# Kernel tuning notes

Measured on AMD Instinct MI355X. Metric: run time of the kernel, lower is better.

The kernel has to match this reference:

```python
import math
import jax, jax.numpy as jnp
import numpy as np

N, E, D, H, NH, DH, EIN, EOUT, G = 30000, 480000, 128, 128, 4, 32, 16, 16, 64
EPS = 1e-5

def _leaky(x):
    return jax.nn.leaky_relu(x, 0.01)

def _graph_norm(x, batch, w, b, a):
    # torch_geometric GraphNorm: out = w * (x - a*mean) / sqrt(var + eps) + b, stats per graph
    cnt = jnp.maximum(jax.ops.segment_sum(jnp.ones((x.shape[0],), x.dtype), batch, num_segments=G), 1.0)[:, None]
    mean = jax.ops.segment_sum(x, batch, num_segments=G) / cnt
    out = x - a * mean[batch]
    var = jax.ops.segment_sum(out * out, batch, num_segments=G) / cnt
    return w * out / jnp.sqrt(var + EPS)[batch] + b

def setup_inputs() -> dict:
    key = jax.random.key(0)
    ks = jax.random.split(key, 24)
    lin = lambda k, di, do: jax.random.normal(k, (di, do), jnp.float32) * 0.02
    z = lambda d: jnp.zeros((d,), jnp.float32)
    o = lambda d: jnp.ones((d,), jnp.float32)
    return {
        "node": jax.random.normal(ks[0], (N, D), jnp.float32),
        "edge": jax.random.normal(ks[1], (E, EIN), jnp.float32),
        "coords": jax.random.normal(ks[2], (N, 3), jnp.float32),
        "Ws": lin(ks[3], D, H), "bs": z(H),
        "Wd": lin(ks[4], D, H), "bd": z(H),
        "Wv": lin(ks[5], D, H), "bv": z(H),
        "We1": lin(ks[6], EIN + 1, H), "be1": z(H),
        "We2": lin(ks[7], H, H), "be2": z(H),
        "Wun": lin(ks[8], H, H), "bun": z(H),
        "Wue": lin(ks[9], H, EOUT), "bue": z(EOUT),
        "Wg": lin(ks[10], 3 * H, H), "bg": z(H),
        "Wf1": lin(ks[11], H, H), "bf1": z(H),
        "Wf2": lin(ks[12], H, H), "bf2": z(H),
        "gn1_w": o(H), "gn1_b": z(H), "gn1_a": o(H),
        "gn2_w": o(H), "gn2_b": z(H), "gn2_a": o(H),
        "edge_index": jax.random.randint(ks[13], (2, E), 0, N),
        "batch": jnp.sort(jax.random.randint(ks[14], (N,), 0, G)),
    }

def reference(node, edge, coords, Ws, bs, Wd, bd, Wv, bv, We1, be1, We2, be2,
              Wun, bun, Wue, bue, Wg, bg, Wf1, bf1, Wf2, bf2,
              gn1_w, gn1_b, gn1_a, gn2_w, gn2_b, gn2_a, edge_index, batch):
    i, j = edge_index[0], edge_index[1]
    src = node @ Ws + bs              # [N,H]
    dst = node @ Wd + bd
    value = node @ Wv + bv
    d = coords[i] - coords[j]
    dist = jnp.sqrt(jnp.sum(d * d, axis=-1, keepdims=True) + 1e-12) * 0.1
    e = jnp.concatenate([edge, dist], axis=-1)            # [E, EIN+1]
    e = _leaky(e @ We1 + be1) @ We2 + be2                   # edge_layer (dropout=identity in eval)
    edge_key = src[j] * e
    edge_result = (dst[i] * edge_key / math.sqrt(DH)).reshape(E, NH, DH)
    scores = jnp.sum(jnp.abs(edge_result), axis=2)         # L1 norm over dh -> [E,NH]
    smax = jax.ops.segment_max(scores, i, num_segments=N)  # scatter softmax over dst nodes
    ex = jnp.exp(scores - smax[i])
    den = jax.ops.segment_sum(ex, i, num_segments=N)
    ew = (ex / den[i])[..., None]                           # [E,NH,1]
    agg = jax.ops.segment_sum(ew * value[j].reshape(E, NH, DH), i, num_segments=N).reshape(N, H)
    node_new = agg @ Wun + bun
    edge_new = edge_result.reshape(E, H) @ Wue + bue
    g = jax.nn.sigmoid(jnp.concatenate([node_new, node, node_new - node], axis=-1) @ Wg + bg)
    n1 = _graph_norm(g * node_new + node, batch, gn1_w, gn1_b, gn1_a)
    fx = _leaky(n1 @ Wf1 + bf1) @ Wf2 + bf2                 # fix_node
    n2 = _graph_norm(g * fx + n1, batch, gn2_w, gn2_b, gn2_a)
    return (n2, edge_new, coords)
```

## Files before the change

kernel.cpp:

```cpp
#include <hip/hip_runtime.h>
#include <hip/hip_bf16.h>

#define NN_ 30000
#define NE_ 480000
#define DIM 128
#define EINF 16
#define EOUTF 16
#define NG 64
#define RSQRT_DH 0.17677669529663687f

typedef unsigned short u16;
typedef __attribute__((ext_vector_type(8))) short short8;
typedef __attribute__((ext_vector_type(8))) unsigned short ushort8v;
typedef __attribute__((ext_vector_type(4))) float floatx4;

#define W_DEG     0
#define W_CUR     30000
#define W_GSUM1   60000
#define W_GSQ1    68192
#define W_GSUM2   76384
#define W_GSQ2    84576
#define W_ZEND    92768
#define W_OFF     92768
#define W_BSUM    122772
#define W_GSTART  122900
#define W_EID     122968
#define W_JC      602968
#define W_SCORES  1082968
#define W_SRCB    3002968
#define W_DSTB    4922968
#define W_VALB    6842968
#define W_A       8762968
#define W_B       12602968
#define W_C       16442968
#define W_WGC     20282968
#define W_WE2B    20315736
#define W_WPROJ   20323928
#define W_WUEB    20455000

static __device__ __forceinline__ u16 f2bf(float x) {
  __hip_bfloat16 h = __float2bfloat16(x);
  return *reinterpret_cast<u16*>(&h);
}
static __device__ __forceinline__ float bf2f(u16 v) {
  unsigned int b = ((unsigned int)v) << 16;
  return __uint_as_float(b);
}

static __device__ __forceinline__ void tile_gn_stats(const float* xsb, int ld,
    const int* bg_s, int row0, int tid,
    float* __restrict__ gsum, float* __restrict__ gsq) {
  int c = tid & 127, half = tid >> 7;
  float sm = 0.f, sq = 0.f;
  int gcur = -1;
  for (int r = 0; r < 16; ++r) {
    int rl = half * 16 + r;
    int row = row0 + rl;
    if (row >= NN_) break;
    int g = bg_s[rl];
    float v = xsb[rl * ld + c];
    if (g != gcur) {
      if (gcur >= 0) {
        atomicAdd(&gsum[gcur * DIM + c], sm);
        atomicAdd(&gsq[gcur * DIM + c], sq);
      }
      gcur = g; sm = 0.f; sq = 0.f;
    }
    sm += v; sq += v * v;
  }
  if (gcur >= 0) {
    atomicAdd(&gsum[gcur * DIM + c], sm);
    atomicAdd(&gsq[gcur * DIM + c], sq);
  }
}

__global__ void setup_kernel(const int* __restrict__ batch, int* __restrict__ gstart,
                             const float* __restrict__ Wg,
                             const float* __restrict__ We2, u16* __restrict__ we2b,
                             const float* __restrict__ Ws, const float* __restrict__ Wd,
                             const float* __restrict__ Wv, const float* __restrict__ Wun,
                             const float* __restrict__ Wf1, const float* __restrict__ Wf2,
                             u16* __restrict__ wfrag,
                             const float* __restrict__ Wue, u16* __restrict__ wueb) {
  int b = blockIdx.x, tid = threadIdx.x;
  if (b == 0) {
    int g = tid;
    if (g <= NG) {
      int lo = 0, hi = NN_;
      while (lo < hi) { int mid = (lo + hi) >> 1; if (batch[mid] < g) lo = mid + 1; else hi = mid; }
      gstart[g] = lo;
    }
  } else if (b < 65) {
    int idx = (b - 1) * 256 + tid;
    int j = idx & 7, lane = (idx >> 3) & 63, s = (idx >> 9) & 3, T = idx >> 11;
    int k = s * 32 + ((lane >> 4) << 3) + j;
    int n = T * 16 + (lane & 15);
    we2b[idx] = f2bf(We2[(size_t)k * DIM + n]);
  } else if (b < 1089) {
    int idx = (b - 65) * 256 + tid;
    int which = idx >> 14;
    int sub = idx & 16383;
    int j = sub & 7, lane = (sub >> 3) & 63, s = (sub >> 9) & 3, T = sub >> 11;
    int k = s * 32 + ((lane >> 4) << 3) + j;
    int n = T * 16 + (lane & 15);
    int mat = which >> 1;
    float w;
    if (mat == 4) w = Wg[(size_t)k * DIM + n] + Wg[(size_t)(256 + k) * DIM + n];
    else if (mat == 5) w = Wg[(size_t)(128 + k) * DIM + n] - Wg[(size_t)(256 + k) * DIM + n];
    else {
      const float* Wsrc = (mat == 0) ? Ws : (mat == 1) ? Wd : (mat == 2) ? Wv
                        : (mat == 3) ? Wun : (mat == 6) ? Wf1 : Wf2;
      w = Wsrc[(size_t)k * DIM + n];
    }
    u16 h = f2bf(w);
    wfrag[(size_t)which * 16384 + sub] = (which & 1) ? f2bf(w - bf2f(h)) : h;
  } else {
    int idx = (b - 1089) * 256 + tid;
    int half = idx >> 12;
    int sub = idx & 4095;
    int j = sub & 7, lane = (sub >> 3) & 63, sG = sub >> 9;
    int k = sG * 32 + ((lane >> 4) << 3) + j;
    int n = lane & 15;
    float w = Wue[(size_t)k * EOUTF + n];
    u16 h = f2bf(w);
    wueb[half * 4096 + sub] = half ? f2bf(w - bf2f(h)) : h;
  }
}

__global__ void deg_kernel(const int* __restrict__ EI, int* __restrict__ deg) {
  int e = blockIdx.x * 256 + threadIdx.x;
  if (e < NE_) atomicAdd(&deg[EI[e]], 1);
}

__global__ void __launch_bounds__(256) proj_kernel(
    const float* __restrict__ node, const u16* __restrict__ wfrag,
    const float* __restrict__ bs, const float* __restrict__ bd,
    const float* __restrict__ bv,
    u16* __restrict__ srcb, u16* __restrict__ dstb, u16* __restrict__ valb) {
  __shared__ __align__(16) u16 ah[32 * 136];
  __shared__ __align__(16) u16 al[32 * 136];
  __shared__ __align__(16) float park[32 * 132];
  int tid = threadIdx.x, row0 = blockIdx.x * 32;
  int r2 = tid >> 3, c16 = (tid & 7) * 16;

  {
    int row = row0 + r2;
    float v[16];
    if (row < NN_) {
#pragma unroll
      for (int q = 0; q < 4; ++q) {
        float4 x = *(const float4*)&node[(size_t)row * DIM + c16 + q * 4];
        v[q * 4 + 0] = x.x; v[q * 4 + 1] = x.y;
        v[q * 4 + 2] = x.z; v[q * 4 + 3] = x.w;
      }
    } else {
#pragma unroll
      for (int q = 0; q < 16; ++q) v[q] = 0.f;
    }
#pragma unroll
    for (int h2 = 0; h2 < 2; ++h2) {
      ushort8v hh, ll;
#pragma unroll
      for (int q = 0; q < 8; ++q) {
        float x = v[h2 * 8 + q];
        u16 h = f2bf(x);
        hh[q] = h;
        ll[q] = f2bf(x - bf2f(h));
      }
      *(ushort8v*)&ah[r2 * 136 + c16 + h2 * 8] = hh;
      *(ushort8v*)&al[r2 * 136 + c16 + h2 * 8] = ll;
    }
  }
  __syncthreads();

  int wv_ = tid >> 6, lane = tid & 63;
  int mtile = wv_ & 1, nhalf = wv_ >> 1;
  int quad = lane >> 4, lrow = lane & 15;
  int m0 = mtile * 16;

  short8 afh[4], afl[4];
#pragma unroll
  for (int s = 0; s < 4; ++s) {
    afh[s] = *(const short8*)&ah[(m0 + lrow) * 136 + s * 32 + quad * 8];
    afl[s] = *(const short8*)&al[(m0 + lrow) * 136 + s * 32 + quad * 8];
  }

  const float* Bt[3] = {bs, bd, bv};
  u16* Yt[3] = {srcb, dstb, valb};
#pragma unroll 1
  for (int g3 = 0; g3 < 3; ++g3) {
    const u16* wh = wfrag + (size_t)(g3 * 2 + 0) * 16384;
    const u16* wl = wfrag + (size_t)(g3 * 2 + 1) * 16384;
    floatx4 dacc[4];
#pragma unroll
    for (int t = 0; t < 4; ++t) dacc[t] = (floatx4){0.f, 0.f, 0.f, 0.f};
#pragma unroll
    for (int s = 0; s < 4; ++s) {
#pragma unroll
      for (int t = 0; t < 4; ++t) {
        int T = nhalf * 4 + t;
        size_t off = (size_t)((T * 4 + s) * 64 + lane) * 8;
        short8 bh = *(const short8*)&wh[off];
        short8 bl = *(const short8*)&wl[off];
        dacc[t] = __builtin_amdgcn_mfma_f32_16x16x32_bf16(afh[s], bh, dacc[t], 0, 0, 0);
        dacc[t] = __builtin_amdgcn_mfma_f32_16x16x32_bf16(afl[s], bh, dacc[t], 0, 0, 0);
        dacc[t] = __builtin_amdgcn_mfma_f32_16x16x32_bf16(afh[s], bl, dacc[t], 0, 0, 0);
      }
    }
#pragma unroll
    for (int t = 0; t < 4; ++t) {
      int col = nhalf * 64 + t * 16 + lrow;
#pragma unroll
      for (int r = 0; r < 4; ++r)
        park[(m0 + quad * 4 + r) * 132 + col] = dacc[t][r];
    }
    __syncthreads();
    {
      int row = row0 + r2;
      if (row < NN_) {
#pragma unroll
        for (int h2 = 0; h2 < 2; ++h2) {
          ushort8v o;
#pragma unroll
          for (int q = 0; q < 8; ++q) {
            float pv = park[r2 * 132 + c16 + h2 * 8 + q] + Bt[g3][c16 + h2 * 8 + q];
            o[q] = f2bf(pv);
          }
          *(ushort8v*)&Yt[g3][(size_t)row * DIM + c16 + h2 * 8] = o;
        }
      }
    }
    __syncthreads();
  }
}

__global__ void __launch_bounds__(256) nnew_gate_kernel(
    const float* __restrict__ AGG, const float* __restrict__ NODE,
    const int* __restrict__ batch, const u16* __restrict__ wfrag,
    const float* __restrict__ bun, const float* __restrict__ bg,
    float* __restrict__ gsum1, float* __restrict__ gsq1,
    float* __restrict__ G, float* __restrict__ X1) {
  __shared__ __align__(16) u16 a_h[32 * 136];
  __shared__ __align__(16) u16 a_l[32 * 136];
  __shared__ __align__(16) u16 n_h[32 * 136];
  __shared__ __align__(16) u16 n_l[32 * 136];
  __shared__ __align__(16) float park[32 * 132];
  __shared__ int bg_s[32];
  int tid = threadIdx.x, row0 = blockIdx.x * 32;
  int r2 = tid >> 3, c16 = (tid & 7) * 16;
  if (tid < 32) bg_s[tid] = (row0 + tid < NN_) ? batch[row0 + tid] : 0;

  {
    int row = row0 + r2;
    float va[16], vn[16];
    if (row < NN_) {
#pragma unroll
      for (int q = 0; q < 4; ++q) {
        float4 xa = *(const float4*)&AGG[(size_t)row * DIM + c16 + q * 4];
        float4 xn = *(const float4*)&NODE[(size_t)row * DIM + c16 + q * 4];
        va[q * 4 + 0] = xa.x; va[q * 4 + 1] = xa.y; va[q * 4 + 2] = xa.z; va[q * 4 + 3] = xa.w;
        vn[q * 4 + 0] = xn.x; vn[q * 4 + 1] = xn.y; vn[q * 4 + 2] = xn.z; vn[q * 4 + 3] = xn.w;
      }
    } else {
#pragma unroll
      for (int q = 0; q < 16; ++q) { va[q] = 0.f; vn[q] = 0.f; }
    }
#pragma unroll
    for (int h2 = 0; h2 < 2; ++h2) {
      ushort8v ah8, al8, nh8, nl8;
#pragma unroll
      for (int q = 0; q < 8; ++q) {
        float x = va[h2 * 8 + q];
        u16 h = f2bf(x); ah8[q] = h; al8[q] = f2bf(x - bf2f(h));
        float y = vn[h2 * 8 + q];
        u16 hy = f2bf(y); nh8[q] = hy; nl8[q] = f2bf(y - bf2f(hy));
      }
      *(ushort8v*)&a_h[r2 * 136 + c16 + h2 * 8] = ah8;
      *(ushort8v*)&a_l[r2 * 136 + c16 + h2 * 8] = al8;
      *(ushort8v*)&n_h[r2 * 136 + c16 + h2 * 8] = nh8;
      *(ushort8v*)&n_l[r2 * 136 + c16 + h2 * 8] = nl8;
    }
  }
  __syncthreads();

  int wv_ = tid >> 6, lane = tid & 63;
  int mtile = wv_ & 1, nhalf = wv_ >> 1;
  int quad = lane >> 4, lrow = lane & 15;
  int m0 = mtile * 16;

  const u16* WunH = wfrag + (size_t)6 * 16384;
  const u16* WunL = wfrag + (size_t)7 * 16384;
  const u16* G0H  = wfrag + (size_t)8 * 16384;
  const u16* G0L  = wfrag + (size_t)9 * 16384;
  const u16* G1H  = wfrag + (size_t)10 * 16384;
  const u16* G1L  = wfrag + (size_t)11 * 16384;

  {
    short8 fh[4], fl[4];
#pragma unroll
    for (int s = 0; s < 4; ++s) {
      fh[s] = *(const short8*)&a_h[(m0 + lrow) * 136 + s * 32 + quad * 8];
      fl[s] = *(const short8*)&a_l[(m0 + lrow) * 136 + s * 32 + quad * 8];
    }
    floatx4 d1[4];
#pragma unroll
    for (int t = 0; t < 4; ++t) d1[t] = (floatx4){0.f, 0.f, 0.f, 0.f};
#pragma unroll
    for (int s = 0; s < 4; ++s) {
#pragma unroll
      for (int t = 0; t < 4; ++t) {
        int T = nhalf * 4 + t;
        size_t off = (size_t)((T * 4 + s) * 64 + lane) * 8;
        short8 bh = *(const short8*)&WunH[off];
        short8 bl = *(const short8*)&WunL[off];
        d1[t] = __builtin_amdgcn_mfma_f32_16x16x32_bf16(fh[s], bh, d1[t], 0, 0, 0);
        d1[t] = __builtin_amdgcn_mfma_f32_16x16x32_bf16(fl[s], bh, d1[t], 0, 0, 0);
        d1[t] = __builtin_amdgcn_mfma_f32_16x16x32_bf16(fh[s], bl, d1[t], 0, 0, 0);
      }
    }
#pragma unroll
    for (int t = 0; t < 4; ++t) {
      int col = nhalf * 64 + t * 16 + lrow;
#pragma unroll
      for (int r = 0; r < 4; ++r)
        park[(m0 + quad * 4 + r) * 132 + col] = d1[t][r];
    }
  }
  __syncthreads();

  {
#pragma unroll
    for (int h2 = 0; h2 < 2; ++h2) {
      ushort8v hh, ll;
#pragma unroll
      for (int q = 0; q < 8; ++q) {
        float x = park[r2 * 132 + c16 + h2 * 8 + q] + bun[c16 + h2 * 8 + q];
        u16 h = f2bf(x); hh[q] = h; ll[q] = f2bf(x - bf2f(h));
      }
      *(ushort8v*)&a_h[r2 * 136 + c16 + h2 * 8] = hh;
      *(ushort8v*)&a_l[r2 * 136 + c16 + h2 * 8] = ll;
    }
  }
  __syncthreads();

  {
    short8 mh[4], ml[4], ph[4], pl[4];
#pragma unroll
    for (int s = 0; s < 4; ++s) {
      mh[s] = *(const short8*)&a_h[(m0 + lrow) * 136 + s * 32 + quad * 8];
      ml[s] = *(const short8*)&a_l[(m0 + lrow) * 136 + s * 32 + quad * 8];
      ph[s] = *(const short8*)&n_h[(m0 + lrow) * 136 + s * 32 + quad * 8];
      pl[s] = *(const short8*)&n_l[(m0 + lrow) * 136 + s * 32 + quad * 8];
    }
    floatx4 d2[4];
#pragma unroll
    for (int t = 0; t < 4; ++t) d2[t] = (floatx4){0.f, 0.f, 0.f, 0.f};
#pragma unroll
    for (int s = 0; s < 4; ++s) {
#pragma unroll
      for (int t = 0; t < 4; ++t) {
        int T = nhalf * 4 + t;
        size_t off = (size_t)((T * 4 + s) * 64 + lane) * 8;
        short8 g0h = *(const short8*)&G0H[off];
        short8 g0l = *(const short8*)&G0L[off];
        short8 g1h = *(const short8*)&G1H[off];
        short8 g1l = *(const short8*)&G1L[off];
        d2[t] = __builtin_amdgcn_mfma_f32_16x16x32_bf16(mh[s], g0h, d2[t], 0, 0, 0);
        d2[t] = __builtin_amdgcn_mfma_f32_16x16x32_bf16(ml[s], g0h, d2[t], 0, 0, 0);
        d2[t] = __builtin_amdgcn_mfma_f32_16x16x32_bf16(mh[s], g0l, d2[t], 0, 0, 0);
        d2[t] = __builtin_amdgcn_mfma_f32_16x16x32_bf16(ph[s], g1h, d2[t], 0, 0, 0);
        d2[t] = __builtin_amdgcn_mfma_f32_16x16x32_bf16(pl[s], g1h, d2[t], 0, 0, 0);
        d2[t] = __builtin_amdgcn_mfma_f32_16x16x32_bf16(ph[s], g1l, d2[t], 0, 0, 0);
      }
    }
#pragma unroll
    for (int t = 0; t < 4; ++t) {
      int col = nhalf * 64 + t * 16 + lrow;
      float bgv = bg[col], bunv = bun[col];
#pragma unroll
      for (int r = 0; r < 4; ++r) {
        int erow = m0 + quad * 4 + r;
        int row = row0 + erow;
        float z = d2[t][r] + bgv;
        float gg = 1.f / (1.f + __expf(-z));
        float nn = park[erow * 132 + col] + bunv;
        float nodev = bf2f(n_h[erow * 136 + col]) + bf2f(n_l[erow * 136 + col]);
        float x1 = gg * nn + nodev;
        park[erow * 132 + col] = x1;
        if (row < NN_) {
          G[(size_t)row * DIM + col] = gg;
          X1[(size_t)row * DIM + col] = x1;
        }
      }
    }
  }
  __syncthreads();
  tile_gn_stats(park, 132, bg_s, row0, tid, gsum1, gsq1);
}

__global__ void __launch_bounds__(256) fx_kernel(
    const float* __restrict__ X1, const int* __restrict__ batch,
    const int* __restrict__ gstart,
    const float* __restrict__ gsum1, const float* __restrict__ gsq1,
    const float* __restrict__ g1w, const float* __restrict__ g1b,
    const float* __restrict__ g1a, const u16* __restrict__ wfrag,
    const float* __restrict__ bf1, const float* __restrict__ bf2,
    const float* __restrict__ G,
    float* __restrict__ gsum2, float* __restrict__ gsq2,
    float* __restrict__ X2) {
  __shared__ __align__(16) u16 a_h[32 * 136];
  __shared__ __align__(16) u16 a_l[32 * 136];
  __shared__ __align__(16) float n1s[32 * 132];
  __shared__ int bg_s[32];
  int tid = threadIdx.x, row0 = blockIdx.x * 32;
  int r2 = tid >> 3, c16 = (tid & 7) * 16;
  if (tid < 32) bg_s[tid] = (row0 + tid < NN_) ? batch[row0 + tid] : 0;

  {
    int row = row0 + r2;
    int gi = (row < NN_) ? batch[row] : 0;
    float cnt = fmaxf((float)(gstart[gi + 1] - gstart[gi]), 1.f);
    float inv = 1.f / cnt;
    float v[16];
    if (row < NN_) {
#pragma unroll
      for (int q = 0; q < 4; ++q) {
        float4 x = *(const float4*)&X1[(size_t)row * DIM + c16 + q * 4];
        v[q * 4 + 0] = x.x; v[q * 4 + 1] = x.y;
        v[q * 4 + 2] = x.z; v[q * 4 + 3] = x.w;
      }
    } else {
#pragma unroll
      for (int q = 0; q < 16; ++q) v[q] = 0.f;
    }
#pragma unroll
    for (int q0 = 0; q0 < 16; ++q0) {
      int c = c16 + q0;
      float sm = gsum1[gi * DIM + c], sq = gsq1[gi * DIM + c];
      float mean = sm * inv, msq = sq * inv, am = g1a[c] * mean;
      float var = msq - 2.f * am * mean + am * am;
      v[q0] = g1w[c] * (v[q0] - am) * rsqrtf(var + 1e-5f) + g1b[c];
    }
#pragma unroll
    for (int q = 0; q < 4; ++q) {
      float4 o; o.x = v[q * 4 + 0]; o.y = v[q * 4 + 1];
      o.z = v[q * 4 + 2]; o.w = v[q * 4 + 3];
      *(float4*)&n1s[r2 * 132 + c16 + q * 4] = o;
    }
#pragma unroll
    for (int h2 = 0; h2 < 2; ++h2) {
      ushort8v hh, ll;
#pragma unroll
      for (int q = 0; q < 8; ++q) {
        float x = v[h2 * 8 + q];
        u16 h = f2bf(x); hh[q] = h; ll[q] = f2bf(x - bf2f(h));
      }
      *(ushort8v*)&a_h[r2 * 136 + c16 + h2 * 8] = hh;
      *(ushort8v*)&a_l[r2 * 136 + c16 + h2 * 8] = ll;
    }
  }
  __syncthreads();

  int wv_ = tid >> 6, lane = tid & 63;
  int mtile = wv_ & 1, nhalf = wv_ >> 1;
  int quad = lane >> 4, lrow = lane & 15;
  int m0 = mtile * 16;

  const u16* F1H = wfrag + (size_t)12 * 16384;
  const u16* F1L = wfrag + (size_t)13 * 16384;
  const u16* F2H = wfrag + (size_t)14 * 16384;
  const u16* F2L = wfrag + (size_t)15 * 16384;

  short8 fh[4], fl[4];
#pragma unroll
  for (int s = 0; s < 4; ++s) {
    fh[s] = *(const short8*)&a_h[(m0 + lrow) * 136 + s * 32 + quad * 8];
    fl[s] = *(const short8*)&a_l[(m0 + lrow) * 136 + s * 32 + quad * 8];
  }
  __syncthreads();

  {
    floatx4 d1[4];
#pragma unroll
    for (int t = 0; t < 4; ++t) d1[t] = (floatx4){0.f, 0.f, 0.f, 0.f};
#pragma unroll
    for (int s = 0; s < 4; ++s) {
#pragma unroll
      for (int t = 0; t < 4; ++t) {
        int T = nhalf * 4 + t;
        size_t off = (size_t)((T * 4 + s) * 64 + lane) * 8;
        short8 bh = *(const short8*)&F1H[off];
        short8 bl = *(const short8*)&F1L[off];
        d1[t] = __builtin_amdgcn_mfma_f32_16x16x32_bf16(fh[s], bh, d1[t], 0, 0, 0);
        d1[t] = __builtin_amdgcn_mfma_f32_16x16x32_bf16(fl[s], bh, d1[t], 0, 0, 0);
        d1[t] = __builtin_amdgcn_mfma_f32_16x16x32_bf16(fh[s], bl, d1[t], 0, 0, 0);
      }
    }
#pragma unroll
    for (int t = 0; t < 4; ++t) {
      int col = nhalf * 64 + t * 16 + lrow;
      float b1v = bf1[col];
#pragma unroll
      for (int r = 0; r < 4; ++r) {
        int erow = m0 + quad * 4 + r;
        float tt = d1[t][r] + b1v;
        tt = tt > 0.f ? tt : 0.01f * tt;
        u16 h = f2bf(tt);
        a_h[erow * 136 + col] = h;
        a_l[erow * 136 + col] = f2bf(tt - bf2f(h));
      }
    }
  }
  __syncthreads();

  {
    short8 th[4], tl[4];
#pragma unroll
    for (int s = 0; s < 4; ++s) {
      th[s] = *(const short8*)&a_h[(m0 + lrow) * 136 + s * 32 + quad * 8];
      tl[s] = *(const short8*)&a_l[(m0 + lrow) * 136 + s * 32 + quad * 8];
    }
    floatx4 d2[4];
#pragma unroll
    for (int t = 0; t < 4; ++t) d2[t] = (floatx4){0.f, 0.f, 0.f, 0.f};
#pragma unroll
    for (int s = 0; s < 4; ++s) {
#pragma unroll
      for (int t = 0; t < 4; ++t) {
        int T = nhalf * 4 + t;
        size_t off = (size_t)((T * 4 + s) * 64 + lane) * 8;
        short8 bh = *(const short8*)&F2H[off];
        short8 bl = *(const short8*)&F2L[off];
        d2[t] = __builtin_amdgcn_mfma_f32_16x16x32_bf16(th[s], bh, d2[t], 0, 0, 0);
        d2[t] = __builtin_amdgcn_mfma_f32_16x16x32_bf16(tl[s], bh, d2[t], 0, 0, 0);
        d2[t] = __builtin_amdgcn_mfma_f32_16x16x32_bf16(th[s], bl, d2[t], 0, 0, 0);
      }
    }
#pragma unroll
    for (int t = 0; t < 4; ++t) {
      int col = nhalf * 64 + t * 16 + lrow;
      float b2v = bf2[col];
#pragma unroll
      for (int r = 0; r < 4; ++r) {
        int erow = m0 + quad * 4 + r;
        int row = row0 + erow;
        float gg = (row < NN_) ? G[(size_t)row * DIM + col] : 0.f;
        float x2 = gg * (d2[t][r] + b2v) + n1s[erow * 132 + col];
        n1s[erow * 132 + col] = x2;
        if (row < NN_) X2[(size_t)row * DIM + col] = x2;
      }
    }
  }
  __syncthreads();
  tile_gn_stats(n1s, 132, bg_s, row0, tid, gsum2, gsq2);
}

__global__ void scanA_kernel(const int* __restrict__ deg, int* __restrict__ off,
                             int* __restrict__ bsum) {
  __shared__ int buf[256];
  int tid = threadIdx.x;
  int i = blockIdx.x * 256 + tid;
  int v = (i < NN_) ? deg[i] : 0;
  buf[tid] = v;
  __syncthreads();
  for (int s = 1; s < 256; s <<= 1) {
    int t = (tid >= s) ? buf[tid - s] : 0;
    __syncthreads();
    buf[tid] += t;
    __syncthreads();
  }
  if (i < NN_) off[i] = buf[tid] - v;
  if (tid == 255) bsum[blockIdx.x] = buf[255];
}

__global__ void scanB_kernel(int* __restrict__ bsum) {
  const int NBLK = (NN_ + 255) / 256;
  __shared__ int buf[128];
  int tid = threadIdx.x;
  int v = (tid < NBLK) ? bsum[tid] : 0;
  buf[tid] = v;
  __syncthreads();
  for (int s = 1; s < 128; s <<= 1) {
    int t = (tid >= s) ? buf[tid - s] : 0;
    __syncthreads();
    buf[tid] += t;
    __syncthreads();
  }
  if (tid < NBLK) bsum[tid] = buf[tid] - v;
}

__global__ void scanC_kernel(int* __restrict__ off, const int* __restrict__ bsum) {
  int i = blockIdx.x * 256 + threadIdx.x;
  if (i < NN_) off[i] += bsum[i >> 8];
  if (i == 0) off[NN_] = NE_;
}

__global__ void fill_kernel(const int* __restrict__ EI, const int* __restrict__ off,
                            int* __restrict__ cur, int* __restrict__ eidb,
                            int* __restrict__ jcsr) {
  int e = blockIdx.x * 256 + threadIdx.x;
  if (e >= NE_) return;
  int i = EI[e];
  int p = atomicAdd(&cur[i], 1);
  int pos = off[i] + p;
  eidb[pos] = e;
  jcsr[pos] = EI[NE_ + e];
}

__global__ void __launch_bounds__(256, 6) edge_kernel(
    const float* __restrict__ edgef, const float* __restrict__ coords,
    const int* __restrict__ EI, const int* __restrict__ eidb,
    const float* __restrict__ We1, const float* __restrict__ be1,
    const float* __restrict__ be2, const u16* __restrict__ we2b,
    const u16* __restrict__ wueb, const float* __restrict__ bue,
    const u16* __restrict__ srcb, const u16* __restrict__ dstb,
    float* __restrict__ scores, float* __restrict__ outE) {
  __shared__ __align__(16) float sbuf[5504];
  __shared__ float bue_s[EOUTF];
  __shared__ int ii[32], jj[32], ee[32];

  float* xs   = sbuf;
  u16*   hbf  = (u16*)(sbuf + 640);
  float* park = sbuf;
  float* ers  = sbuf + 1280;

  int tid = threadIdx.x;
  int bid = blockIdx.x;
  int bswz = (bid & 7) * (NE_ / 32 / 8) + (bid >> 3);
  int p0 = bswz * 32;

  if (tid < 32) {
    int p = p0 + tid;
    int e = eidb[p];
    ee[tid] = e;
    int i = EI[e], j = EI[NE_ + e];
    ii[tid] = i; jj[tid] = j;
    float dx = coords[i * 3 + 0] - coords[j * 3 + 0];
    float dy = coords[i * 3 + 1] - coords[j * 3 + 1];
    float dz = coords[i * 3 + 2] - coords[j * 3 + 2];
    float dist = sqrtf(dx * dx + dy * dy + dz * dz + 1e-12f) * 0.1f;
    xs[tid * 20 + 16] = dist;
  }
  if (tid < EOUTF) bue_s[tid] = bue[tid];
  __syncthreads();

  if (tid < 128) {
    int r = tid >> 2, c4 = (tid & 3) * 4;
    *(float4*)&xs[r * 20 + c4] = *(const float4*)&edgef[(size_t)ee[r] * EINF + c4];
  }
  __syncthreads();

  int cg = tid & 31, rg = tid >> 5, c0 = cg * 4, r0 = rg * 4;

  {
    float acc[4][4] = {};
    for (int k = 0; k < 16; k += 4) {
      float4 w0 = *(const float4*)&We1[(size_t)(k + 0) * DIM + c0];
      float4 w1 = *(const float4*)&We1[(size_t)(k + 1) * DIM + c0];
      float4 w2 = *(const float4*)&We1[(size_t)(k + 2) * DIM + c0];
      float4 w3 = *(const float4*)&We1[(size_t)(k + 3) * DIM + c0];
#pragma unroll
      for (int u = 0; u < 4; ++u) {
        float4 xv = *(const float4*)&xs[(r0 + u) * 20 + k];
        acc[u][0] += xv.x * w0.x + xv.y * w1.x + xv.z * w2.x + xv.w * w3.x;
        acc[u][1] += xv.x * w0.y + xv.y * w1.y + xv.z * w2.y + xv.w * w3.y;
        acc[u][2] += xv.x * w0.z + xv.y * w1.z + xv.z * w2.z + xv.w * w3.z;
        acc[u][3] += xv.x * w0.w + xv.y * w1.w + xv.z * w2.w + xv.w * w3.w;
      }
    }
    {
      float4 w4 = *(const float4*)&We1[(size_t)16 * DIM + c0];
#pragma unroll
      for (int u = 0; u < 4; ++u) {
        float xd = xs[(r0 + u) * 20 + 16];
        acc[u][0] += xd * w4.x; acc[u][1] += xd * w4.y;
        acc[u][2] += xd * w4.z; acc[u][3] += xd * w4.w;
      }
    }
    float4 b1 = *(const float4*)&be1[c0];
#pragma unroll
    for (int u = 0; u < 4; ++u) {
      float h0 = acc[u][0] + b1.x, h1 = acc[u][1] + b1.y;
      float h2 = acc[u][2] + b1.z, h3 = acc[u][3] + b1.w;
      h0 = h0 > 0.f ? h0 : 0.01f * h0; h1 = h1 > 0.f ? h1 : 0.01f * h1;
      h2 = h2 > 0.f ? h2 : 0.01f * h2; h3 = h3 > 0.f ? h3 : 0.01f * h3;
      ushort4 pk; pk.x = f2bf(h0); pk.y = f2bf(h1); pk.z = f2bf(h2); pk.w = f2bf(h3);
      *(ushort4*)&hbf[(r0 + u) * 136 + c0] = pk;
    }
  }
  __syncthreads();

  int wv = tid >> 6, lane = tid & 63;
  int mtile = wv & 1, nhalf = wv >> 1;
  int quad = lane >> 4, lrow = lane & 15;
  int m0 = mtile * 16;

  short8 afrag[4];
#pragma unroll
  for (int s = 0; s < 4; ++s)
    afrag[s] = *(const short8*)&hbf[(m0 + lrow) * 136 + s * 32 + quad * 8];
  __syncthreads();

  floatx4 dacc[4];
#pragma unroll
  for (int t = 0; t < 4; ++t) dacc[t] = (floatx4){0.f, 0.f, 0.f, 0.f};
#pragma unroll
  for (int s = 0; s < 4; ++s) {
#pragma unroll
    for (int t = 0; t < 4; ++t) {
      int T = nhalf * 4 + t;
      short8 bfrg = *(const short8*)&we2b[(size_t)((T * 4 + s) * 64 + lane) * 8];
      dacc[t] = __builtin_amdgcn_mfma_f32_16x16x32_bf16(afrag[s], bfrg, dacc[t], 0, 0, 0);
    }
  }

#pragma unroll
  for (int t = 0; t < 4; ++t) {
    int col = nhalf * 64 + t * 16 + lrow;
    float b2v = be2[col];
#pragma unroll
    for (int r = 0; r < 4; ++r) {
      int erow = m0 + quad * 4 + r;
      ers[erow * 132 + col] = dacc[t][r] + b2v;
    }
  }
  __syncthreads();

  {
    int el2 = tid >> 3, cb2 = tid & 7;
    int c0b = cb2 * 16;
    int irow = ii[el2], jrow = jj[el2];
    ushort8v dv8a = *(const ushort8v*)&dstb[(size_t)irow * DIM + c0b];
    ushort8v dv8b = *(const ushort8v*)&dstb[(size_t)irow * DIM + c0b + 8];
    ushort8v sv8a = *(const ushort8v*)&srcb[(size_t)jrow * DIM + c0b];
    ushort8v sv8b = *(const ushort8v*)&srcb[(size_t)jrow * DIM + c0b + 8];

    float ef[16];
#pragma unroll
    for (int q = 0; q < 4; ++q) {
      float4 v = *(const float4*)&ers[el2 * 132 + c0b + q * 4];
      ef[q * 4 + 0] = v.x; ef[q * 4 + 1] = v.y;
      ef[q * 4 + 2] = v.z; ef[q * 4 + 3] = v.w;
    }
    float asum = 0.f;
#pragma unroll
    for (int k = 0; k < 8; ++k) {
      float er = bf2f((u16)dv8a[k]) * bf2f((u16)sv8a[k]) * ef[k] * RSQRT_DH;
      ef[k] = er; asum += fabsf(er);
    }
#pragma unroll
    for (int k = 0; k < 8; ++k) {
      float er = bf2f((u16)dv8b[k]) * bf2f((u16)sv8b[k]) * ef[8 + k] * RSQRT_DH;
      ef[8 + k] = er; asum += fabsf(er);
    }
#pragma unroll
    for (int q = 0; q < 4; ++q) {
      float4 v; v.x = ef[q * 4 + 0]; v.y = ef[q * 4 + 1];
      v.z = ef[q * 4 + 2]; v.w = ef[q * 4 + 3];
      *(float4*)&ers[el2 * 132 + c0b + q * 4] = v;
    }
    asum += __shfl_xor(asum, 1);
    if ((cb2 & 1) == 0)
      scores[(size_t)(p0 + el2) * 4 + (cb2 >> 1)] = asum;
  }
  __syncthreads();

  {
    floatx4 d3 = (floatx4){0.f, 0.f, 0.f, 0.f};
#pragma unroll
    for (int s = 0; s < 2; ++s) {
      int kbase = nhalf * 64 + s * 32 + quad * 8;
      const float* src = &ers[(m0 + lrow) * 132 + kbase];
      float4 e0 = *(const float4*)&src[0];
      float4 e1 = *(const float4*)&src[4];
      float ev[8] = {e0.x, e0.y, e0.z, e0.w, e1.x, e1.y, e1.z, e1.w};
      short8 ah8, al8;
#pragma unroll
      for (int q = 0; q < 8; ++q) {
        u16 h = f2bf(ev[q]);
        ah8[q] = (short)h;
        al8[q] = (short)f2bf(ev[q] - bf2f(h));
      }
      int sG = nhalf * 2 + s;
      size_t off = (size_t)(sG * 64 + lane) * 8;
      short8 bh = *(const short8*)&wueb[off];
      short8 bl = *(const short8*)&wueb[4096 + off];
      d3 = __builtin_amdgcn_mfma_f32_16x16x32_bf16(ah8, bh, d3, 0, 0, 0);
      d3 = __builtin_amdgcn_mfma_f32_16x16x32_bf16(al8, bh, d3, 0, 0, 0);
      d3 = __builtin_amdgcn_mfma_f32_16x16x32_bf16(ah8, bl, d3, 0, 0, 0);
    }
#pragma unroll
    for (int r = 0; r < 4; ++r)
      park[nhalf * 640 + (m0 + quad * 4 + r) * 20 + lrow] = d3[r];
  }
  __syncthreads();

  {
    int el = tid >> 3, oc2 = (tid & 7) * 2;
    float a0 = park[el * 20 + oc2]     + park[640 + el * 20 + oc2]     + bue_s[oc2];
    float a1 = park[el * 20 + oc2 + 1] + park[640 + el * 20 + oc2 + 1] + bue_s[oc2 + 1];
    size_t ob = (size_t)ee[el] * EOUTF + oc2;
    float2 o2; o2.x = a0; o2.y = a1;
    *(float2*)&outE[ob] = o2;
  }
}

__global__ void __launch_bounds__(256) agg_kernel(
    const u16* __restrict__ valb, const float* __restrict__ scores,
    const int* __restrict__ off, const int* __restrict__ jcsr,
    float* __restrict__ agg) {
  int n = blockIdx.x * 4 + (threadIdx.x >> 6);
  int l = threadIdx.x & 63;
  if (n >= NN_) return;
  int s = off[n], e_end = off[n + 1];

  float m0 = -1e30f, m1 = -1e30f, m2 = -1e30f, m3 = -1e30f;
  for (int p = s + l; p < e_end; p += 64) {
    float4 sc = *(const float4*)&scores[(size_t)p * 4];
    m0 = fmaxf(m0, sc.x); m1 = fmaxf(m1, sc.y);
    m2 = fmaxf(m2, sc.z); m3 = fmaxf(m3, sc.w);
  }
#pragma unroll
  for (int d = 1; d < 64; d <<= 1) {
    m0 = fmaxf(m0, __shfl_xor(m0, d)); m1 = fmaxf(m1, __shfl_xor(m1, d));
    m2 = fmaxf(m2, __shfl_xor(m2, d)); m3 = fmaxf(m3, __shfl_xor(m3, d));
  }
  int hh = l >> 4;
  float mh = (hh == 0) ? m0 : (hh == 1) ? m1 : (hh == 2) ? m2 : m3;

  float acc0 = 0.f, acc1 = 0.f, den = 0.f;
  int p = s;
  for (; p + 8 <= e_end; p += 8) {
    int jA[8];
    float sA[8];
    ushort2 uA[8];
#pragma unroll
    for (int q = 0; q < 8; ++q) jA[q] = jcsr[p + q];
#pragma unroll
    for (int q = 0; q < 8; ++q) sA[q] = scores[(size_t)(p + q) * 4 + hh];
#pragma unroll
    for (int q = 0; q < 8; ++q)
      uA[q] = *(const ushort2*)&valb[(size_t)jA[q] * DIM + 2 * l];
#pragma unroll
    for (int q = 0; q < 8; ++q) {
      float e = __expf(sA[q] - mh);
      den += e;
      acc0 += e * bf2f(uA[q].x);
      acc1 += e * bf2f(uA[q].y);
    }
  }
  for (; p + 2 <= e_end; p += 2) {
    int j0 = jcsr[p], j1 = jcsr[p + 1];
    float s0 = scores[(size_t)p * 4 + hh];
    float s1 = scores[(size_t)(p + 1) * 4 + hh];
    ushort2 u0 = *(const ushort2*)&valb[(size_t)j0 * DIM + 2 * l];
    ushort2 u1 = *(const ushort2*)&valb[(size_t)j1 * DIM + 2 * l];
    float e0 = __expf(s0 - mh), e1 = __expf(s1 - mh);
    den += e0 + e1;
    acc0 += e0 * bf2f(u0.x) + e1 * bf2f(u1.x);
    acc1 += e0 * bf2f(u0.y) + e1 * bf2f(u1.y);
  }
  if (p < e_end) {
    int j = jcsr[p];
    float s0 = scores[(size_t)p * 4 + hh];
    ushort2 u0 = *(const ushort2*)&valb[(size_t)j * DIM + 2 * l];
    float e0 = __expf(s0 - mh);
    den += e0;
    acc0 += e0 * bf2f(u0.x);
    acc1 += e0 * bf2f(u0.y);
  }
  float2 o;
  if (e_end > s) { o.x = acc0 / den; o.y = acc1 / den; }
  else { o.x = 0.f; o.y = 0.f; }
  *(float2*)&agg[(size_t)n * DIM + 2 * l] = o;
}

__global__ void gn_apply_kernel(const float* __restrict__ X, const int* __restrict__ batch,
    const int* __restrict__ gstart, const float* __restrict__ gsum,
    const float* __restrict__ gsq, const float* __restrict__ w,
    const float* __restrict__ b, const float* __restrict__ a,
    float* __restrict__ Y,
    const float* __restrict__ C, float* __restrict__ OC) {
  int blk = blockIdx.x;
  if (blk >= (NN_ * 32) / 256) {
    int i = (blk - (NN_ * 32) / 256) * 256 + threadIdx.x;
    if (i < NN_ * 3) OC[i] = C[i];
    return;
  }
  int idx = blk * 256 + threadIdx.x;
  int n = idx >> 5, c4 = (idx & 31) * 4;
  int g = batch[n];
  float cnt = fmaxf((float)(gstart[g + 1] - gstart[g]), 1.f);
  float inv = 1.f / cnt;
  float4 xv = *(const float4*)&X[(size_t)n * DIM + c4];
  float4 sm = *(const float4*)&gsum[g * DIM + c4];
  float4 sq = *(const float4*)&gsq[g * DIM + c4];
  float4 av = *(const float4*)&a[c4];
  float4 wv = *(const float4*)&w[c4];
  float4 bv = *(const float4*)&b[c4];
  float4 ov;
  {
    float mean = sm.x * inv, msq = sq.x * inv, am = av.x * mean;
    float var = msq - 2.f * am * mean + am * am;
    ov.x = wv.x * (xv.x - am) * rsqrtf(var + 1e-5f) + bv.x;
  }
  {
    float mean = sm.y * inv, msq = sq.y * inv, am = av.y * mean;
    float var = msq - 2.f * am * mean + am * am;
    ov.y = wv.y * (xv.y - am) * rsqrtf(var + 1e-5f) + bv.y;
  }
  {
    float mean = sm.z * inv, msq = sq.z * inv, am = av.z * mean;
    float var = msq - 2.f * am * mean + am * am;
    ov.z = wv.z * (xv.z - am) * rsqrtf(var + 1e-5f) + bv.z;
  }
  {
    float mean = sm.w * inv, msq = sq.w * inv, am = av.w * mean;
    float var = msq - 2.f * am * mean + am * am;
    ov.w = wv.w * (xv.w - am) * rsqrtf(var + 1e-5f) + bv.w;
  }
  *(float4*)&Y[(size_t)n * DIM + c4] = ov;
}

extern "C" void kernel_launch(void* const* d_in, const int* in_sizes, int n_in,
                              void* d_out, int out_size, void* d_ws, size_t ws_size,
                              hipStream_t stream) {
  (void)in_sizes; (void)n_in; (void)out_size; (void)ws_size;
  const float* node  = (const float*)d_in[0];
  const float* edgef = (const float*)d_in[1];
  const float* coords= (const float*)d_in[2];
  const float* Ws  = (const float*)d_in[3];  const float* bs  = (const float*)d_in[4];
  const float* Wd  = (const float*)d_in[5];  const float* bd  = (const float*)d_in[6];
  const float* Wv  = (const float*)d_in[7];  const float* bv  = (const float*)d_in[8];
  const float* We1 = (const float*)d_in[9];  const float* be1 = (const float*)d_in[10];
  const float* We2 = (const float*)d_in[11]; const float* be2 = (const float*)d_in[12];
  const float* Wun = (const float*)d_in[13]; const float* bun = (const float*)d_in[14];
  const float* Wue = (const float*)d_in[15]; const float* bue = (const float*)d_in[16];
  const float* Wg  = (const float*)d_in[17]; const float* bg  = (const float*)d_in[18];
  const float* Wf1 = (const float*)d_in[19]; const float* bf1 = (const float*)d_in[20];
  const float* Wf2 = (const float*)d_in[21]; const float* bf2 = (const float*)d_in[22];
  const float* g1w = (const float*)d_in[23]; const float* g1b = (const float*)d_in[24];
  const float* g1a = (const float*)d_in[25];
  const float* g2w = (const float*)d_in[26]; const float* g2b = (const float*)d_in[27];
  const float* g2a = (const float*)d_in[28];
  const int* EI    = (const int*)d_in[29];
  const int* batch = (const int*)d_in[30];
  float* out = (float*)d_out;

  int*   wsi = (int*)d_ws;
  float* wsf = (float*)d_ws;
  int* deg    = wsi + W_DEG;
  int* cur    = wsi + W_CUR;
  int* offs   = wsi + W_OFF;
  int* bsum   = wsi + W_BSUM;
  int* gstart = wsi + W_GSTART;
  int* eidb   = wsi + W_EID;
  int* jcsr   = wsi + W_JC;
  float* gsum1 = wsf + W_GSUM1; float* gsq1 = wsf + W_GSQ1;
  float* gsum2 = wsf + W_GSUM2; float* gsq2 = wsf + W_GSQ2;
  float* scores_ = wsf + W_SCORES;
  u16* srcb = (u16*)(wsf + W_SRCB);
  u16* dstb = (u16*)(wsf + W_DSTB);
  u16* valb = (u16*)(wsf + W_VALB);
  float* A = wsf + W_A;
  float* B = wsf + W_B;
  u16*   we2b  = (u16*)(wsf + W_WE2B);
  u16*   wfrag = (u16*)(wsf + W_WPROJ);
  u16*   wueb  = (u16*)(wsf + W_WUEB);

  float* outE = out + (size_t)NN_ * DIM;
  float* outC = out + (size_t)NN_ * DIM + (size_t)NE_ * EOUTF;

  hipMemsetAsync(d_ws, 0, (size_t)W_ZEND * sizeof(int), stream);
  setup_kernel<<<1121, 256, 0, stream>>>(batch, gstart, Wg, We2, we2b,
                                         Ws, Wd, Wv, Wun, Wf1, Wf2, wfrag,
                                         Wue, wueb);
  deg_kernel<<<(NE_ + 255) / 256, 256, 0, stream>>>(EI, deg);
  scanA_kernel<<<(NN_ + 255) / 256, 256, 0, stream>>>(deg, offs, bsum);
  scanB_kernel<<<1, 128, 0, stream>>>(bsum);
  scanC_kernel<<<(NN_ + 255) / 256, 256, 0, stream>>>(offs, bsum);
  fill_kernel<<<(NE_ + 255) / 256, 256, 0, stream>>>(EI, offs, cur, eidb, jcsr);
  proj_kernel<<<(NN_ + 31) / 32, 256, 0, stream>>>(node, wfrag, bs, bd, bv,
                                                   srcb, dstb, valb);
  edge_kernel<<<NE_ / 32, 256, 0, stream>>>(edgef, coords, EI, eidb, We1, be1,
                                            be2, we2b, wueb, bue,
                                            srcb, dstb, scores_, outE);
  agg_kernel<<<NN_ / 4, 256, 0, stream>>>(valb, scores_, offs, jcsr, A);
  nnew_gate_kernel<<<(NN_ + 31) / 32, 256, 0, stream>>>(A, node, batch, wfrag,
                                                        bun, bg, gsum1, gsq1, B, A);
  fx_kernel<<<(NN_ + 31) / 32, 256, 0, stream>>>(A, batch, gstart, gsum1, gsq1,
                                                 g1w, g1b, g1a, wfrag, bf1, bf2,
                                                 B, gsum2, gsq2, A);
  gn_apply_kernel<<<(NN_ * 32) / 256 + (NN_ * 3 + 255) / 256, 256, 0, stream>>>(
      A, batch, gstart, gsum2, gsq2, g2w, g2b, g2a, out, coords, outC);
}
```

Baseline: 516.6 us.

## Fuse softmax aggregation into node gate kernel and merge degree count into setup

Removes the separate aggregation kernel. Each thread of the node update kernel now runs the scatter-softmax and weighted value gather for its row and 16 columns directly, and feeds the result into the MFMA input staging. This drops the write and re-read of the 30000x128 fp32 aggregate and one launch. The per-edge degree atomics are also folded into the setup kernel as extra blocks. In exchange, each thread walks its whole edge list serially with only 8 threads per row, which lowers the parallelism of the gather compared with the 64-lane per-node kernel and may expose latency.

```diff
diff --git a/kernel.cpp b/kernel.cpp
--- a/kernel.cpp
+++ b/kernel.cpp
@@ -81,7 +81,8 @@
                              const float* __restrict__ Wv, const float* __restrict__ Wun,
                              const float* __restrict__ Wf1, const float* __restrict__ Wf2,
                              u16* __restrict__ wfrag,
-                             const float* __restrict__ Wue, u16* __restrict__ wueb) {
+                             const float* __restrict__ Wue, u16* __restrict__ wueb,
+                             const int* __restrict__ EI, int* __restrict__ deg) {
   int b = blockIdx.x, tid = threadIdx.x;
   if (b == 0) {
     int g = tid;
@@ -114,7 +115,7 @@
     }
     u16 h = f2bf(w);
     wfrag[(size_t)which * 16384 + sub] = (which & 1) ? f2bf(w - bf2f(h)) : h;
-  } else {
+  } else if (b < 1121) {
     int idx = (b - 1089) * 256 + tid;
     int half = idx >> 12;
     int sub = idx & 4095;
@@ -124,12 +125,10 @@
     float w = Wue[(size_t)k * EOUTF + n];
     u16 h = f2bf(w);
     wueb[half * 4096 + sub] = half ? f2bf(w - bf2f(h)) : h;
-  }
-}
-
-__global__ void deg_kernel(const int* __restrict__ EI, int* __restrict__ deg) {
-  int e = blockIdx.x * 256 + threadIdx.x;
-  if (e < NE_) atomicAdd(&deg[EI[e]], 1);
+  } else {
+    int e = (b - 1121) * 256 + tid;
+    if (e < NE_) atomicAdd(&deg[EI[e]], 1);
+  }
 }
 
 __global__ void __launch_bounds__(256) proj_kernel(
@@ -235,7 +234,9 @@
 }
 
 __global__ void __launch_bounds__(256) nnew_gate_kernel(
-    const float* __restrict__ AGG, const float* __restrict__ NODE,
+    const u16* __restrict__ valb, const float* __restrict__ scores,
+    const int* __restrict__ off, const int* __restrict__ jcsr,
+    const float* __restrict__ NODE,
     const int* __restrict__ batch, const u16* __restrict__ wfrag,
     const float* __restrict__ bun, const float* __restrict__ bg,
     float* __restrict__ gsum1, float* __restrict__ gsq1,
@@ -252,25 +253,70 @@
 
   {
     int row = row0 + r2;
-    float va[16], vn[16];
+    float acc[16];
+#pragma unroll
+    for (int q = 0; q < 16; ++q) acc[q] = 0.f;
     if (row < NN_) {
+      int s = off[row], e_end = off[row + 1];
+      if (e_end > s) {
+        int head = c16 >> 5;
+        float m = -1e30f;
+        for (int p = s; p < e_end; ++p)
+          m = fmaxf(m, scores[(size_t)p * 4 + head]);
+        float den = 0.f;
+        int p = s;
+        for (; p + 2 <= e_end; p += 2) {
+          int j0 = jcsr[p], j1 = jcsr[p + 1];
+          float s0 = scores[(size_t)p * 4 + head];
+          float s1 = scores[(size_t)(p + 1) * 4 + head];
+          ushort8v v00 = *(const ushort8v*)&valb[(size_t)j0 * DIM + c16];
+          ushort8v v01 = *(const ushort8v*)&valb[(size_t)j0 * DIM + c16 + 8];
+          ushort8v v10 = *(const ushort8v*)&valb[(size_t)j1 * DIM + c16];
+          ushort8v v11 = *(const ushort8v*)&valb[(size_t)j1 * DIM + c16 + 8];
+          float e0 = __expf(s0 - m), e1 = __expf(s1 - m);
+          den += e0 + e1;
+#pragma unroll
+          for (int q = 0; q < 8; ++q) {
+            acc[q]     += e0 * bf2f(v00[q]) + e1 * bf2f(v10[q]);
+            acc[8 + q] += e0 * bf2f(v01[q]) + e1 * bf2f(v11[q]);
+          }
+        }
+        if (p < e_end) {
+          int j = jcsr[p];
+          float s0 = scores[(size_t)p * 4 + head];
+          ushort8v v0 = *(const ushort8v*)&valb[(size_t)j * DIM + c16];
+          ushort8v v1 = *(const ushort8v*)&valb[(size_t)j * DIM + c16 + 8];
+          float e0 = __expf(s0 - m);
+          den += e0;
+#pragma unroll
+          for (int q = 0; q < 8; ++q) {
+            acc[q]     += e0 * bf2f(v0[q]);
+            acc[8 + q] += e0 * bf2f(v1[q]);
+          }
+        }
+        float inv = 1.f / den;
+#pragma unroll
+        for (int q = 0; q < 16; ++q) acc[q] *= inv;
+      }
+    }
+    float vn[16];
+    if (row < NN_) {
 #pragma unroll
       for (int q = 0; q < 4; ++q) {
-        float4 xa = *(const float4*)&AGG[(size_t)row * DIM + c16 + q * 4];
         float4 xn = *(const float4*)&NODE[(size_t)row * DIM + c16 + q * 4];
-        va[q * 4 + 0] = xa.x; va[q * 4 + 1] = xa.y; va[q * 4 + 2] = xa.z; va[q * 4 + 3] = xa.w;
-        vn[q * 4 + 0] = xn.x; vn[q * 4 + 1] = xn.y; vn[q * 4 + 2] = xn.z; vn[q * 4 + 3] = xn.w;
+        vn[q * 4 + 0] = xn.x; vn[q * 4 + 1] = xn.y;
+        vn[q * 4 + 2] = xn.z; vn[q * 4 + 3] = xn.w;
       }
     } else {
 #pragma unroll
-      for (int q = 0; q < 16; ++q) { va[q] = 0.f; vn[q] = 0.f; }
+      for (int q = 0; q < 16; ++q) vn[q] = 0.f;
     }
 #pragma unroll
     for (int h2 = 0; h2 < 2; ++h2) {
       ushort8v ah8, al8, nh8, nl8;
 #pragma unroll
       for (int q = 0; q < 8; ++q) {
-        float x = va[h2 * 8 + q];
+        float x = acc[h2 * 8 + q];
         u16 h = f2bf(x); ah8[q] = h; al8[q] = f2bf(x - bf2f(h));
         float y = vn[h2 * 8 + q];
         u16 hy = f2bf(y); nh8[q] = hy; nl8[q] = f2bf(y - bf2f(hy));
@@ -310,9 +356,9 @@
 #pragma unroll
       for (int t = 0; t < 4; ++t) {
         int T = nhalf * 4 + t;
-        size_t off = (size_t)((T * 4 + s) * 64 + lane) * 8;
-        short8 bh = *(const short8*)&WunH[off];
-        short8 bl = *(const short8*)&WunL[off];
+        size_t off2 = (size_t)((T * 4 + s) * 64 + lane) * 8;
+        short8 bh = *(const short8*)&WunH[off2];
+        short8 bl = *(const short8*)&WunL[off2];
         d1[t] = __builtin_amdgcn_mfma_f32_16x16x32_bf16(fh[s], bh, d1[t], 0, 0, 0);
         d1[t] = __builtin_amdgcn_mfma_f32_16x16x32_bf16(fl[s], bh, d1[t], 0, 0, 0);
         d1[t] = __builtin_amdgcn_mfma_f32_16x16x32_bf16(fh[s], bl, d1[t], 0, 0, 0);
@@ -360,11 +406,11 @@
 #pragma unroll
       for (int t = 0; t < 4; ++t) {
         int T = nhalf * 4 + t;
-        size_t off = (size_t)((T * 4 + s) * 64 + lane) * 8;
-        short8 g0h = *(const short8*)&G0H[off];
-        short8 g0l = *(const short8*)&G0L[off];
-        short8 g1h = *(const short8*)&G1H[off];
-        short8 g1l = *(const short8*)&G1L[off];
+        size_t off2 = (size_t)((T * 4 + s) * 64 + lane) * 8;
+        short8 g0h = *(const short8*)&G0H[off2];
+        short8 g0l = *(const short8*)&G0L[off2];
+        short8 g1h = *(const short8*)&G1H[off2];
+        short8 g1l = *(const short8*)&G1L[off2];
         d2[t] = __builtin_amdgcn_mfma_f32_16x16x32_bf16(mh[s], g0h, d2[t], 0, 0, 0);
         d2[t] = __builtin_amdgcn_mfma_f32_16x16x32_bf16(ml[s], g0h, d2[t], 0, 0, 0);
         d2[t] = __builtin_amdgcn_mfma_f32_16x16x32_bf16(mh[s], g0l, d2[t], 0, 0, 0);
@@ -488,9 +534,9 @@
 #pragma unroll
       for (int t = 0; t < 4; ++t) {
         int T = nhalf * 4 + t;
-        size_t off = (size_t)((T * 4 + s) * 64 + lane) * 8;
-        short8 bh = *(const short8*)&F1H[off];
-        short8 bl = *(const short8*)&F1L[off];
+        size_t off2 = (size_t)((T * 4 + s) * 64 + lane) * 8;
+        short8 bh = *(const short8*)&F1H[off2];
+        short8 bl = *(const short8*)&F1L[off2];
         d1[t] = __builtin_amdgcn_mfma_f32_16x16x32_bf16(fh[s], bh, d1[t], 0, 0, 0);
         d1[t] = __builtin_amdgcn_mfma_f32_16x16x32_bf16(fl[s], bh, d1[t], 0, 0, 0);
         d1[t] = __builtin_amdgcn_mfma_f32_16x16x32_bf16(fh[s], bl, d1[t], 0, 0, 0);
@@ -528,9 +574,9 @@
 #pragma unroll
       for (int t = 0; t < 4; ++t) {
         int T = nhalf * 4 + t;
-        size_t off = (size_t)((T * 4 + s) * 64 + lane) * 8;
-        short8 bh = *(const short8*)&F2H[off];
-        short8 bl = *(const short8*)&F2L[off];
+        size_t off2 = (size_t)((T * 4 + s) * 64 + lane) * 8;
+        short8 bh = *(const short8*)&F2H[off2];
+        short8 bl = *(const short8*)&F2L[off2];
         d2[t] = __builtin_amdgcn_mfma_f32_16x16x32_bf16(th[s], bh, d2[t], 0, 0, 0);
         d2[t] = __builtin_amdgcn_mfma_f32_16x16x32_bf16(tl[s], bh, d2[t], 0, 0, 0);
         d2[t] = __builtin_amdgcn_mfma_f32_16x16x32_bf16(th[s], bl, d2[t], 0, 0, 0);
@@ -803,76 +849,6 @@
     float2 o2; o2.x = a0; o2.y = a1;
     *(float2*)&outE[ob] = o2;
   }
-}
-
-__global__ void __launch_bounds__(256) agg_kernel(
-    const u16* __restrict__ valb, const float* __restrict__ scores,
-    const int* __restrict__ off, const int* __restrict__ jcsr,
-    float* __restrict__ agg) {
-  int n = blockIdx.x * 4 + (threadIdx.x >> 6);
-  int l = threadIdx.x & 63;
-  if (n >= NN_) return;
-  int s = off[n], e_end = off[n + 1];
-
-  float m0 = -1e30f, m1 = -1e30f, m2 = -1e30f, m3 = -1e30f;
-  for (int p = s + l; p < e_end; p += 64) {
-    float4 sc = *(const float4*)&scores[(size_t)p * 4];
-    m0 = fmaxf(m0, sc.x); m1 = fmaxf(m1, sc.y);
-    m2 = fmaxf(m2, sc.z); m3 = fmaxf(m3, sc.w);
-  }
-#pragma unroll
-  for (int d = 1; d < 64; d <<= 1) {
-    m0 = fmaxf(m0, __shfl_xor(m0, d)); m1 = fmaxf(m1, __shfl_xor(m1, d));
-    m2 = fmaxf(m2, __shfl_xor(m2, d)); m3 = fmaxf(m3, __shfl_xor(m3, d));
-  }
-  int hh = l >> 4;
-  float mh = (hh == 0) ? m0 : (hh == 1) ? m1 : (hh == 2) ? m2 : m3;
-
-  float acc0 = 0.f, acc1 = 0.f, den = 0.f;
-  int p = s;
-  for (; p + 8 <= e_end; p += 8) {
-    int jA[8];
-    float sA[8];
-    ushort2 uA[8];
-#pragma unroll
-    for (int q = 0; q < 8; ++q) jA[q] = jcsr[p + q];
-#pragma unroll
-    for (int q = 0; q < 8; ++q) sA[q] = scores[(size_t)(p + q) * 4 + hh];
-#pragma unroll
-    for (int q = 0; q < 8; ++q)
-      uA[q] = *(const ushort2*)&valb[(size_t)jA[q] * DIM + 2 * l];
-#pragma unroll
-    for (int q = 0; q < 8; ++q) {
-      float e = __expf(sA[q] - mh);
-      den += e;
-      acc0 += e * bf2f(uA[q].x);
-      acc1 += e * bf2f(uA[q].y);
-    }
-  }
-  for (; p + 2 <= e_end; p += 2) {
-    int j0 = jcsr[p], j1 = jcsr[p + 1];
-    float s0 = scores[(size_t)p * 4 + hh];
-    float s1 = scores[(size_t)(p + 1) * 4 + hh];
-    ushort2 u0 = *(const ushort2*)&valb[(size_t)j0 * DIM + 2 * l];
-    ushort2 u1 = *(const ushort2*)&valb[(size_t)j1 * DIM + 2 * l];
-    float e0 = __expf(s0 - mh), e1 = __expf(s1 - mh);
-    den += e0 + e1;
-    acc0 += e0 * bf2f(u0.x) + e1 * bf2f(u1.x);
-    acc1 += e0 * bf2f(u0.y) + e1 * bf2f(u1.y);
-  }
-  if (p < e_end) {
-    int j = jcsr[p];
-    float s0 = scores[(size_t)p * 4 + hh];
-    ushort2 u0 = *(const ushort2*)&valb[(size_t)j * DIM + 2 * l];
-    float e0 = __expf(s0 - mh);
-    den += e0;
-    acc0 += e0 * bf2f(u0.x);
-    acc1 += e0 * bf2f(u0.y);
-  }
-  float2 o;
-  if (e_end > s) { o.x = acc0 / den; o.y = acc1 / den; }
-  else { o.x = 0.f; o.y = 0.f; }
-  *(float2*)&agg[(size_t)n * DIM + 2 * l] = o;
 }
 
 __global__ void gn_apply_kernel(const float* __restrict__ X, const int* __restrict__ batch,
@@ -972,10 +948,9 @@
   float* outC = out + (size_t)NN_ * DIM + (size_t)NE_ * EOUTF;
 
   hipMemsetAsync(d_ws, 0, (size_t)W_ZEND * sizeof(int), stream);
-  setup_kernel<<<1121, 256, 0, stream>>>(batch, gstart, Wg, We2, we2b,
-                                         Ws, Wd, Wv, Wun, Wf1, Wf2, wfrag,
-                                         Wue, wueb);
-  deg_kernel<<<(NE_ + 255) / 256, 256, 0, stream>>>(EI, deg);
+  setup_kernel<<<1121 + (NE_ + 255) / 256, 256, 0, stream>>>(
+      batch, gstart, Wg, We2, we2b, Ws, Wd, Wv, Wun, Wf1, Wf2, wfrag,
+      Wue, wueb, EI, deg);
   scanA_kernel<<<(NN_ + 255) / 256, 256, 0, stream>>>(deg, offs, bsum);
   scanB_kernel<<<1, 128, 0, stream>>>(bsum);
   scanC_kernel<<<(NN_ + 255) / 256, 256, 0, stream>>>(offs, bsum);
@@ -985,9 +960,9 @@
   edge_kernel<<<NE_ / 32, 256, 0, stream>>>(edgef, coords, EI, eidb, We1, be1,
                                             be2, we2b, wueb, bue,
                                             srcb, dstb, scores_, outE);
-  agg_kernel<<<NN_ / 4, 256, 0, stream>>>(valb, scores_, offs, jcsr, A);
-  nnew_gate_kernel<<<(NN_ + 31) / 32, 256, 0, stream>>>(A, node, batch, wfrag,
-                                                        bun, bg, gsum1, gsq1, B, A);
+  nnew_gate_kernel<<<(NN_ + 31) / 32, 256, 0, stream>>>(
+      valb, scores_, offs, jcsr, node, batch, wfrag, bun, bg,
+      gsum1, gsq1, B, A);
   fx_kernel<<<(NN_ + 31) / 32, 256, 0, stream>>>(A, batch, gstart, gsum1, gsq1,
                                                  g1w, g1b, g1a, wfrag, bf1, bf2,
                                                  B, gsum2, gsq2, A);
```

New measurement: 508.6 us. Within noise of the previous version (-1.5%).
